# Kernel tuning notes

Hardware: AMD Instinct MI355X
Metric: run time of the kernel (lower is better)

The kernel has to match this reference:

```python
import jax, jax.numpy as jnp
import numpy as np

B, S, H = 4, 2048, 1024   # batch, seq_len, hidden_dim
E, D = 8, 1024            # num_experts, expert_dim (== hidden per module structure)
TOP_K = 2


def setup_inputs() -> dict:
    key = jax.random.key(0)
    ks = jax.random.split(key, 8)
    scale_h = 1.0 / np.sqrt(H)
    scale_d = 1.0 / np.sqrt(D)
    return {
        "x": jax.random.normal(ks[0], (B, S, H), dtype=jnp.float32),
        # router linear: hidden -> num_experts
        "w_router": jax.random.normal(ks[1], (H, E), dtype=jnp.float32) * scale_h,
        "b_router": jnp.zeros((E,), dtype=jnp.float32),
        # per-expert linear: hidden -> expert_dim
        "w_experts": jax.random.normal(ks[2], (E, H, D), dtype=jnp.float32) * scale_h,
        "b_experts": jnp.zeros((E, D), dtype=jnp.float32),
        # output linear: expert_dim -> expert_dim
        "w_out": jax.random.normal(ks[3], (D, D), dtype=jnp.float32) * scale_d,
        "b_out": jnp.zeros((D,), dtype=jnp.float32),
    }


def reference(x, w_router, b_router, w_experts, b_experts, w_out, b_out):
    # --- MoERouter: softmax over expert logits, top-2, renormalize ---
    logits = jnp.einsum("bsh,he->bse", x, w_router) + b_router          # [B,S,E]
    probs = jax.nn.softmax(logits, axis=-1)
    top_p, top_i = jax.lax.top_k(probs, TOP_K)                           # [B,S,2]
    top_p = top_p / jnp.sum(top_p, axis=-1, keepdims=True)
    # --- Dense expert compute over all tokens (module computes every expert) ---
    expert_out = jnp.einsum("bsh,ehd->bsed", x, w_experts) + b_experts   # [B,S,E,D]
    expert_out = jax.nn.gelu(expert_out)
    # --- Gather top-2 expert outputs and combine with routing weights ---
    sel = jnp.take_along_axis(expert_out, top_i[..., None], axis=2)      # [B,S,2,D]
    combined = jnp.sum(sel * top_p[..., None], axis=2)                   # [B,S,D]
    # --- Output projection ---
    return jnp.einsum("bsd,de->bse", combined, w_out) + b_out
```

## Files before the change

kernel.cpp:

```cpp
#include <hip/hip_runtime.h>


#define TOKENS 8192
#define HDIM   1024
#define DDIM   1024
#define NEXP   8

typedef __bf16 bf16x8 __attribute__((ext_vector_type(8)));
typedef float  f32x4  __attribute__((ext_vector_type(4)));

__device__ __forceinline__ unsigned short f2b(float f) {
  unsigned int u = __builtin_bit_cast(unsigned int, f);
  u = u + 0x7fffu + ((u >> 16) & 1u);
  return (unsigned short)(u >> 16);
}
__device__ __forceinline__ float b2f(unsigned short b) {
  unsigned int u = ((unsigned int)b) << 16;
  return __builtin_bit_cast(float, u);
}

__device__ __forceinline__ void gld_lds16(const void* g, void* l) {
  __builtin_amdgcn_global_load_lds(
      (__attribute__((address_space(1))) void*)(g),
      (__attribute__((address_space(3))) void*)(l),
      16, 0, 0);
}


__global__ void transpose_cvt_kernel(const float* __restrict__ we, const float* __restrict__ wo,
                                     unsigned short* __restrict__ weT, unsigned short* __restrict__ woT) {
  __shared__ unsigned short tile[32][33];
  int z = blockIdx.z;
  const float* s;
  unsigned short* d;
  if (z < 8) { s = we + (size_t)z * HDIM * DDIM; d = weT + (size_t)z * HDIM * DDIM; }
  else       { s = wo;                            d = woT; }
  int bx = blockIdx.x * 32;
  int by = blockIdx.y * 32;
  for (int i = threadIdx.y; i < 32; i += 8)
    tile[i][threadIdx.x] = f2b(s[(size_t)(by + i) * 1024 + bx + threadIdx.x]);
  __syncthreads();
  for (int i = threadIdx.y; i < 32; i += 8)
    d[(size_t)(bx + i) * 1024 + by + threadIdx.x] = tile[threadIdx.x][i];
}


__global__ void router_compute_kernel(const float* __restrict__ x, const float* __restrict__ wr,
                                      const float* __restrict__ br,
                                      int* __restrict__ eidx, float* __restrict__ ew,
                                      unsigned short* __restrict__ xb) {
  int wave = threadIdx.x >> 6, lane = threadIdx.x & 63;
  int t = blockIdx.x * 4 + wave;
  const float* xp = x + (size_t)t * HDIM;
  unsigned short* xbp = xb + (size_t)t * HDIM;
  float acc[8];
#pragma unroll
  for (int e = 0; e < 8; ++e) acc[e] = 0.f;
#pragma unroll
  for (int h0 = 0; h0 < HDIM; h0 += 256) {
    int h = h0 + lane * 4;
    float4 xv = *(const float4*)&xp[h];
    ushort4 o;
    o.x = f2b(xv.x); o.y = f2b(xv.y); o.z = f2b(xv.z); o.w = f2b(xv.w);
    *(ushort4*)&xbp[h] = o;
    float xq[4] = {xv.x, xv.y, xv.z, xv.w};
#pragma unroll
    for (int q = 0; q < 4; ++q) {
      const float4* wp = (const float4*)&wr[(h + q) * 8];
      float4 w0 = wp[0], w1 = wp[1];
      acc[0] += xq[q] * w0.x; acc[1] += xq[q] * w0.y; acc[2] += xq[q] * w0.z; acc[3] += xq[q] * w0.w;
      acc[4] += xq[q] * w1.x; acc[5] += xq[q] * w1.y; acc[6] += xq[q] * w1.z; acc[7] += xq[q] * w1.w;
    }
  }
#pragma unroll
  for (int off = 32; off; off >>= 1)
#pragma unroll
    for (int e = 0; e < 8; ++e) acc[e] += __shfl_xor(acc[e], off, 64);
  if (lane == 0) {
    float l[8], p[8];
    float m = -1e30f;
#pragma unroll
    for (int e = 0; e < 8; ++e) { l[e] = acc[e] + br[e]; m = fmaxf(m, l[e]); }
    float s = 0.f;
#pragma unroll
    for (int e = 0; e < 8; ++e) { p[e] = __expf(l[e] - m); s += p[e]; }
    int i1 = 0;
#pragma unroll
    for (int e = 1; e < 8; ++e) if (p[e] > p[i1]) i1 = e;
    int i2 = (i1 == 0) ? 1 : 0;
#pragma unroll
    for (int e = 0; e < 8; ++e) if (e != i1 && p[e] > p[i2]) i2 = e;
    float ps = p[i1] + p[i2];
    eidx[t * 2]     = i1;  ew[t * 2]     = p[i1] / ps;
    eidx[t * 2 + 1] = i2;  ew[t * 2 + 1] = p[i2] / ps;
  }
}


__global__ __launch_bounds__(1024) void build_lists_kernel(
    const int* __restrict__ eidx, const float* __restrict__ ew,
    int* __restrict__ counts, int* __restrict__ tok2, float* __restrict__ wl) {
  int e = blockIdx.x;
  int tid = threadIdx.x;
  int lane = tid & 63, wv = tid >> 6;
  __shared__ int wsum[16];
  __shared__ int base;
  if (tid == 0) base = 0;
  __syncthreads();
  for (int c = 0; c < 2 * TOKENS; c += 1024) {
    int i = c + tid;
    bool m = (eidx[i] == e);
    unsigned long long bal = __ballot(m);
    if (lane == 0) wsum[wv] = __popcll(bal);
    __syncthreads();
    int wbase = base;
    for (int w = 0; w < wv; ++w) wbase += wsum[w];
    if (m) {
      int pos = wbase + __popcll(bal & ((1ull << lane) - 1ull));
      tok2[e * TOKENS + pos] = i;
      wl[e * TOKENS + pos] = ew[i];
    }
    int total = 0;
#pragma unroll
    for (int w = 0; w < 16; ++w) total += wsum[w];
    __syncthreads();
    if (tid == 0) base += total;
    __syncthreads();
  }
  if (tid == 0) counts[e] = base;
}


__global__ __launch_bounds__(256, 4) void expert_gemm_kernel(
    const unsigned short* __restrict__ xb, const unsigned short* __restrict__ weT,
    const float* __restrict__ b_experts, const int* __restrict__ counts,
    const int* __restrict__ tok2, const float* __restrict__ wlist,
    unsigned short* __restrict__ outslot) {
  int b = blockIdx.x;
  int id = (b >> 3) + (b & 7) * 512;
  int e = id >> 9;
  int rem = id & 511;
  int m0 = (rem >> 3) << 7;
  int n0 = (rem & 7) << 7;
  int cnt = counts[e];
  if (m0 >= cnt) return;

  __shared__ unsigned short As[2][128 * 32];
  __shared__ unsigned short Bs[2][128 * 32];
  __shared__ int   tokS[128];
  __shared__ float wS[128];

  int tid = threadIdx.x;
  if (tid < 128) {
    int r = m0 + tid;
    tokS[tid] = (r < cnt) ? tok2[e * TOKENS + r] : 0;
    wS[tid]   = (r < cnt) ? wlist[e * TOKENS + r] : 0.f;
  }
  __syncthreads();

  int wave = tid >> 6, lane = tid & 63;
  int subr = lane >> 2, koff = (lane & 3) * 8;

  const unsigned short* wbase = weT + (size_t)e * (HDIM * DDIM);
  const unsigned short* asrc[2];
  const unsigned short* bsrc[2];
  unsigned short* adst[2][2];
  unsigned short* bdst[2][2];
#pragma unroll
  for (int i = 0; i < 2; ++i) {
    int row = i * 64 + wave * 16 + subr;
    asrc[i] = xb + (size_t)(tokS[row] >> 1) * HDIM + koff;
    bsrc[i] = wbase + (size_t)(n0 + row) * HDIM + koff;
#pragma unroll
    for (int bb = 0; bb < 2; ++bb) {
      adst[bb][i] = &As[bb][i * 2048 + wave * 512];
      bdst[bb][i] = &Bs[bb][i * 2048 + wave * 512];
    }
  }

  int wm = wave & 1, wn = wave >> 1;
  int quad = lane >> 4, lr = lane & 15;

  f32x4 zero = {0.f, 0.f, 0.f, 0.f};
  f32x4 acc[4][4];
#pragma unroll
  for (int i = 0; i < 4; ++i)
#pragma unroll
    for (int j = 0; j < 4; ++j) acc[i][j] = zero;

#pragma unroll
  for (int i = 0; i < 2; ++i) {
    gld_lds16(asrc[i], adst[0][i]);
    gld_lds16(bsrc[i], bdst[0][i]);
  }

#pragma unroll 2
  for (int kk = 0; kk < 32; ++kk) {
    __syncthreads();
    if (kk < 31) {
      int off = (kk + 1) * 32;
      int nb = (kk + 1) & 1;
#pragma unroll
      for (int i = 0; i < 2; ++i) {
        gld_lds16(asrc[i] + off, adst[nb][i]);
        gld_lds16(bsrc[i] + off, bdst[nb][i]);
      }
    }
    int cb = kk & 1;
    bf16x8 af[4], bfr[4];
#pragma unroll
    for (int i = 0; i < 4; ++i)
      af[i] = *(const bf16x8*)&As[cb][(wm * 64 + i * 16 + lr) * 32 + quad * 8];
#pragma unroll
    for (int j = 0; j < 4; ++j)
      bfr[j] = *(const bf16x8*)&Bs[cb][(wn * 64 + j * 16 + lr) * 32 + quad * 8];
#pragma unroll
    for (int i = 0; i < 4; ++i)
#pragma unroll
      for (int j = 0; j < 4; ++j)
        acc[i][j] = __builtin_amdgcn_mfma_f32_16x16x32_bf16(af[i], bfr[j], acc[i][j], 0, 0, 0);
  }

#pragma unroll
  for (int j = 0; j < 4; ++j) {
    int col = n0 + wn * 64 + j * 16 + lr;
    float bias = b_experts[e * DDIM + col];
#pragma unroll
    for (int i = 0; i < 4; ++i) {
      int rbase = wm * 64 + i * 16 + quad * 4;
#pragma unroll
      for (int r = 0; r < 4; ++r) {
        int row = rbase + r;
        if (m0 + row < cnt) {
          float h = acc[i][j][r] + bias;
          float z = 0.7978845608f * (h + 0.044715f * h * h * h);
          float t = 1.f - 2.f / (__expf(2.f * z) + 1.f);
          float g = 0.5f * h * (1.f + t);
          outslot[(size_t)tokS[row] * DDIM + col] = f2b(g * wS[row]);
        }
      }
    }
  }
}


__global__ void combine_kernel(const ushort4* __restrict__ outslot, ushort4* __restrict__ comb) {
  int i = blockIdx.x * 256 + threadIdx.x;
  int t = i >> 8, d4 = i & 255;
  ushort4 a = outslot[t * 512 + d4];
  ushort4 b = outslot[t * 512 + 256 + d4];
  ushort4 o;
  o.x = f2b(b2f(a.x) + b2f(b.x));
  o.y = f2b(b2f(a.y) + b2f(b.y));
  o.z = f2b(b2f(a.z) + b2f(b.z));
  o.w = f2b(b2f(a.w) + b2f(b.w));
  comb[i] = o;
}


__global__ __launch_bounds__(256, 4) void out_gemm_kernel(
    const unsigned short* __restrict__ Abf, const unsigned short* __restrict__ BT,
    const float* __restrict__ bias, float* __restrict__ out) {
  int b = blockIdx.x;
  int id = (b >> 3) + (b & 7) * 64;
  int n0 = (id >> 6) << 7;
  int m0 = (id & 63) << 7;

  __shared__ unsigned short As[2][128 * 32];
  __shared__ unsigned short Bs[2][128 * 32];
  int tid = threadIdx.x, wave = tid >> 6, lane = tid & 63;
  int subr = lane >> 2, koff = (lane & 3) * 8;

  const unsigned short* asrc[2];
  const unsigned short* bsrc[2];
  unsigned short* adst[2][2];
  unsigned short* bdst[2][2];
#pragma unroll
  for (int i = 0; i < 2; ++i) {
    int row = i * 64 + wave * 16 + subr;
    asrc[i] = Abf + (size_t)(m0 + row) * DDIM + koff;
    bsrc[i] = BT + (size_t)(n0 + row) * DDIM + koff;
#pragma unroll
    for (int bb = 0; bb < 2; ++bb) {
      adst[bb][i] = &As[bb][i * 2048 + wave * 512];
      bdst[bb][i] = &Bs[bb][i * 2048 + wave * 512];
    }
  }

  int wm = wave & 1, wn = wave >> 1;
  int quad = lane >> 4, lr = lane & 15;

  f32x4 zero = {0.f, 0.f, 0.f, 0.f};
  f32x4 acc[4][4];
#pragma unroll
  for (int i = 0; i < 4; ++i)
#pragma unroll
    for (int j = 0; j < 4; ++j) acc[i][j] = zero;

#pragma unroll
  for (int i = 0; i < 2; ++i) {
    gld_lds16(asrc[i], adst[0][i]);
    gld_lds16(bsrc[i], bdst[0][i]);
  }

#pragma unroll 2
  for (int kk = 0; kk < 32; ++kk) {
    __syncthreads();
    if (kk < 31) {
      int off = (kk + 1) * 32;
      int nb = (kk + 1) & 1;
#pragma unroll
      for (int i = 0; i < 2; ++i) {
        gld_lds16(asrc[i] + off, adst[nb][i]);
        gld_lds16(bsrc[i] + off, bdst[nb][i]);
      }
    }
    int cb = kk & 1;
    bf16x8 af[4], bfr[4];
#pragma unroll
    for (int i = 0; i < 4; ++i)
      af[i] = *(const bf16x8*)&As[cb][(wm * 64 + i * 16 + lr) * 32 + quad * 8];
#pragma unroll
    for (int j = 0; j < 4; ++j)
      bfr[j] = *(const bf16x8*)&Bs[cb][(wn * 64 + j * 16 + lr) * 32 + quad * 8];
#pragma unroll
    for (int i = 0; i < 4; ++i)
#pragma unroll
      for (int j = 0; j < 4; ++j)
        acc[i][j] = __builtin_amdgcn_mfma_f32_16x16x32_bf16(af[i], bfr[j], acc[i][j], 0, 0, 0);
  }

#pragma unroll
  for (int j = 0; j < 4; ++j) {
    int col = n0 + wn * 64 + j * 16 + lr;
    float bs = bias[col];
#pragma unroll
    for (int i = 0; i < 4; ++i) {
      int rbase = wm * 64 + i * 16 + quad * 4;
#pragma unroll
      for (int r = 0; r < 4; ++r)
        out[(size_t)(m0 + rbase + r) * DDIM + col] = acc[i][j][r] + bs;
    }
  }
}


extern "C" void kernel_launch(void* const* d_in, const int* in_sizes, int n_in,
                              void* d_out, int out_size, void* d_ws, size_t ws_size,
                              hipStream_t stream) {
  const float* x  = (const float*)d_in[0];
  const float* wr = (const float*)d_in[1];
  const float* br = (const float*)d_in[2];
  const float* we = (const float*)d_in[3];
  const float* be = (const float*)d_in[4];
  const float* wo = (const float*)d_in[5];
  const float* bo = (const float*)d_in[6];
  float* out = (float*)d_out;

  char* ws = (char*)d_ws;
  unsigned short* xb      = (unsigned short*)(ws);
  unsigned short* weT     = (unsigned short*)(ws + 16777216);
  unsigned short* woT     = (unsigned short*)(ws + 33554432);
  unsigned short* outslot = (unsigned short*)(ws + 35651584);
  int*            counts  = (int*)           (ws + 69206016);
  int*            tok2    = (int*)           (ws + 69206272);
  float*          wlist   = (float*)         (ws + 69468416);
  int*            eidx    = (int*)           (ws + 69730560);
  float*          ew      = (float*)         (ws + 69796096);
  unsigned short* comb    = xb;

  router_compute_kernel<<<2048, 256, 0, stream>>>(x, wr, br, eidx, ew, xb);
  transpose_cvt_kernel<<<dim3(32, 32, 9), dim3(32, 8), 0, stream>>>(we, wo, weT, woT);
  build_lists_kernel<<<8, 1024, 0, stream>>>(eidx, ew, counts, tok2, wlist);
  expert_gemm_kernel<<<4096, 256, 0, stream>>>(xb, weT, be, counts, tok2, wlist, outslot);
  combine_kernel<<<8192, 256, 0, stream>>>((const ushort4*)outslot, (ushort4*)comb);
  out_gemm_kernel<<<512, 256, 0, stream>>>(comb, woT, bo, out);
}
```

Baseline: 286.6 us.

## Triple-buffer LDS tiles with explicit vmcnt waits in both GEMM kernels

Both GEMM kernels move from double-buffered to triple-buffered LDS staging. Two k-tiles are prefetched ahead, and __syncthreads is replaced with a partial s_waitcnt vmcnt(4) plus a raw s_barrier, so one tile's loads can stay in flight while the current tile is computed. The main loop is fully unrolled so the modulo-3 buffer indices become constants. In exchange, LDS per block grows to about 48 KB, and launch bounds drop from 4 to 3 blocks per CU, which lowers occupancy. Correctness now depends on the hand-tuned vmcnt count matching the number of outstanding LDS-direct loads.

```diff
diff --git a/kernel.cpp b/kernel.cpp
--- a/kernel.cpp
+++ b/kernel.cpp
@@ -131,7 +131,7 @@
 }
 
 
-__global__ __launch_bounds__(256, 4) void expert_gemm_kernel(
+__global__ __launch_bounds__(256, 3) void expert_gemm_kernel(
     const unsigned short* __restrict__ xb, const unsigned short* __restrict__ weT,
     const float* __restrict__ b_experts, const int* __restrict__ counts,
     const int* __restrict__ tok2, const float* __restrict__ wlist,
@@ -145,8 +145,8 @@
   int cnt = counts[e];
   if (m0 >= cnt) return;
 
-  __shared__ unsigned short As[2][128 * 32];
-  __shared__ unsigned short Bs[2][128 * 32];
+  __shared__ unsigned short As[3][128 * 32];
+  __shared__ unsigned short Bs[3][128 * 32];
   __shared__ int   tokS[128];
   __shared__ float wS[128];
 
@@ -164,15 +164,15 @@
   const unsigned short* wbase = weT + (size_t)e * (HDIM * DDIM);
   const unsigned short* asrc[2];
   const unsigned short* bsrc[2];
-  unsigned short* adst[2][2];
-  unsigned short* bdst[2][2];
+  unsigned short* adst[3][2];
+  unsigned short* bdst[3][2];
 #pragma unroll
   for (int i = 0; i < 2; ++i) {
     int row = i * 64 + wave * 16 + subr;
     asrc[i] = xb + (size_t)(tokS[row] >> 1) * HDIM + koff;
     bsrc[i] = wbase + (size_t)(n0 + row) * HDIM + koff;
 #pragma unroll
-    for (int bb = 0; bb < 2; ++bb) {
+    for (int bb = 0; bb < 3; ++bb) {
       adst[bb][i] = &As[bb][i * 2048 + wave * 512];
       bdst[bb][i] = &Bs[bb][i * 2048 + wave * 512];
     }
@@ -189,24 +189,28 @@
     for (int j = 0; j < 4; ++j) acc[i][j] = zero;
 
 #pragma unroll
-  for (int i = 0; i < 2; ++i) {
-    gld_lds16(asrc[i], adst[0][i]);
-    gld_lds16(bsrc[i], bdst[0][i]);
-  }
-
-#pragma unroll 2
+  for (int s = 0; s < 2; ++s)
+#pragma unroll
+    for (int i = 0; i < 2; ++i) {
+      gld_lds16(asrc[i] + s * 32, adst[s][i]);
+      gld_lds16(bsrc[i] + s * 32, bdst[s][i]);
+    }
+
+#pragma unroll
   for (int kk = 0; kk < 32; ++kk) {
-    __syncthreads();
-    if (kk < 31) {
-      int off = (kk + 1) * 32;
-      int nb = (kk + 1) & 1;
+    if (kk < 31) asm volatile("s_waitcnt vmcnt(4)" ::: "memory");
+    else         asm volatile("s_waitcnt vmcnt(0)" ::: "memory");
+    __builtin_amdgcn_s_barrier();
+    if (kk + 2 < 32) {
+      int nb = (kk + 2) % 3;
+      int off = (kk + 2) * 32;
 #pragma unroll
       for (int i = 0; i < 2; ++i) {
         gld_lds16(asrc[i] + off, adst[nb][i]);
         gld_lds16(bsrc[i] + off, bdst[nb][i]);
       }
     }
-    int cb = kk & 1;
+    int cb = kk % 3;
     bf16x8 af[4], bfr[4];
 #pragma unroll
     for (int i = 0; i < 4; ++i)
@@ -258,7 +262,7 @@
 }
 
 
-__global__ __launch_bounds__(256, 4) void out_gemm_kernel(
+__global__ __launch_bounds__(256, 3) void out_gemm_kernel(
     const unsigned short* __restrict__ Abf, const unsigned short* __restrict__ BT,
     const float* __restrict__ bias, float* __restrict__ out) {
   int b = blockIdx.x;
@@ -266,22 +270,22 @@
   int n0 = (id >> 6) << 7;
   int m0 = (id & 63) << 7;
 
-  __shared__ unsigned short As[2][128 * 32];
-  __shared__ unsigned short Bs[2][128 * 32];
+  __shared__ unsigned short As[3][128 * 32];
+  __shared__ unsigned short Bs[3][128 * 32];
   int tid = threadIdx.x, wave = tid >> 6, lane = tid & 63;
   int subr = lane >> 2, koff = (lane & 3) * 8;
 
   const unsigned short* asrc[2];
   const unsigned short* bsrc[2];
-  unsigned short* adst[2][2];
-  unsigned short* bdst[2][2];
+  unsigned short* adst[3][2];
+  unsigned short* bdst[3][2];
 #pragma unroll
   for (int i = 0; i < 2; ++i) {
     int row = i * 64 + wave * 16 + subr;
     asrc[i] = Abf + (size_t)(m0 + row) * DDIM + koff;
     bsrc[i] = BT + (size_t)(n0 + row) * DDIM + koff;
 #pragma unroll
-    for (int bb = 0; bb < 2; ++bb) {
+    for (int bb = 0; bb < 3; ++bb) {
       adst[bb][i] = &As[bb][i * 2048 + wave * 512];
       bdst[bb][i] = &Bs[bb][i * 2048 + wave * 512];
     }
@@ -298,24 +302,28 @@
     for (int j = 0; j < 4; ++j) acc[i][j] = zero;
 
 #pragma unroll
-  for (int i = 0; i < 2; ++i) {
-    gld_lds16(asrc[i], adst[0][i]);
-    gld_lds16(bsrc[i], bdst[0][i]);
-  }
-
-#pragma unroll 2
+  for (int s = 0; s < 2; ++s)
+#pragma unroll
+    for (int i = 0; i < 2; ++i) {
+      gld_lds16(asrc[i] + s * 32, adst[s][i]);
+      gld_lds16(bsrc[i] + s * 32, bdst[s][i]);
+    }
+
+#pragma unroll
   for (int kk = 0; kk < 32; ++kk) {
-    __syncthreads();
-    if (kk < 31) {
-      int off = (kk + 1) * 32;
-      int nb = (kk + 1) & 1;
+    if (kk < 31) asm volatile("s_waitcnt vmcnt(4)" ::: "memory");
+    else         asm volatile("s_waitcnt vmcnt(0)" ::: "memory");
+    __builtin_amdgcn_s_barrier();
+    if (kk + 2 < 32) {
+      int nb = (kk + 2) % 3;
+      int off = (kk + 2) * 32;
 #pragma unroll
       for (int i = 0; i < 2; ++i) {
         gld_lds16(asrc[i] + off, adst[nb][i]);
         gld_lds16(bsrc[i] + off, bdst[nb][i]);
       }
     }
-    int cb = kk & 1;
+    int cb = kk % 3;
     bf16x8 af[4], bfr[4];
 #pragma unroll
     for (int i = 0; i < 4; ++i)
```

Result: faster. 280.0 us (-2.3%).
